# Optimization experiments

Measured on AMD Instinct MI355X. Metric: run time of the kernel, lower is better.

Reference implementation:

```python
import jax, jax.numpy as jnp
import numpy as np

HIDDEN = 450
DEPTH = 4
ATOM_FDIM = 35
BOND_FDIM = 5
MAX_NB = 15
N_ATOMS = 30000
N_BONDS = 60000
N_MESS = 10001
N_MOLS = 1000
EPS = 1e-5


def setup_inputs() -> dict:
    key = jax.random.key(0)
    ks = jax.random.split(key, 10)
    fatoms = jax.random.normal(ks[0], (N_ATOMS, ATOM_FDIM), dtype=jnp.float32)
    fbonds = jax.random.normal(ks[1], (N_BONDS, ATOM_FDIM + BOND_FDIM), dtype=jnp.float32)
    # indices into concatenated [tree_message; graph_message] table (index 0 = zero pad slot)
    agraph = jax.random.randint(ks[2], (N_ATOMS, MAX_NB), 0, N_MESS + N_BONDS)
    bgraph = jax.random.randint(ks[3], (N_BONDS, MAX_NB), 0, N_MESS + N_BONDS)
    per_mol = N_ATOMS // N_MOLS
    starts = jnp.arange(N_MOLS, dtype=jnp.int64) * per_mol
    lens = jnp.full((N_MOLS,), per_mol, dtype=jnp.int64)
    scope = jnp.stack([starts, lens], axis=1)
    tree_message = jax.random.normal(ks[4], (N_MESS, HIDDEN), dtype=jnp.float32)
    tree_message = tree_message.at[0].set(0.0)  # padding row
    s = 0.05
    W_i = jax.random.normal(ks[5], (HIDDEN, ATOM_FDIM + BOND_FDIM), dtype=jnp.float32) * s
    W_h = jax.random.normal(ks[6], (HIDDEN, HIDDEN), dtype=jnp.float32) * s
    W_o = jax.random.normal(ks[7], (HIDDEN, ATOM_FDIM + HIDDEN), dtype=jnp.float32) * s
    b_o = jax.random.normal(ks[8], (HIDDEN,), dtype=jnp.float32) * s
    gamma = jnp.ones((HIDDEN,), dtype=jnp.float32)
    beta = jnp.zeros((HIDDEN,), dtype=jnp.float32)
    return {"fatoms": fatoms, "fbonds": fbonds, "agraph": agraph, "bgraph": bgraph,
            "scope": scope, "tree_message": tree_message, "W_i": W_i, "W_h": W_h,
            "W_o": W_o, "b_o": b_o, "gamma": gamma, "beta": beta}


def reference(fatoms, fbonds, agraph, bgraph, scope, tree_message, W_i, W_h, W_o, b_o, gamma, beta):
    # bond input features -> hidden
    binput = fbonds @ W_i.T                      # [n_bonds, H]
    graph_message = jax.nn.relu(binput)
    # message-passing loop (dropout is identity in eval / p=0)
    for _ in range(DEPTH - 1):
        message = jnp.concatenate([tree_message, graph_message], axis=0)
        nei = message[bgraph].sum(axis=1)        # padded-neighbor gather + sum -> [n_bonds, H]
        graph_message = jax.nn.relu(binput + nei @ W_h.T)
    message = jnp.concatenate([tree_message, graph_message], axis=0)
    nei = message[agraph].sum(axis=1)            # [n_atoms, H]
    ainput = jnp.concatenate([fatoms, nei], axis=1)
    h = ainput @ W_o.T + b_o                     # [n_atoms, H]
    # BatchNorm1d (training-mode batch statistics, biased variance)
    mean = h.mean(axis=0)
    var = ((h - mean) ** 2).mean(axis=0)
    h = (h - mean) * jax.lax.rsqrt(var + EPS) * gamma + beta
    h = jax.nn.relu(h)
    # scope-based segment mean pooling
    starts = scope[:, 0]
    lens = scope[:, 1]
    mol_id = jnp.searchsorted(starts, jnp.arange(N_ATOMS), side="right") - 1
    sums = jax.ops.segment_sum(h, mol_id, num_segments=N_MOLS)
    denom = jnp.maximum(lens, 1).astype(h.dtype)[:, None]
    return jnp.where(lens[:, None] > 0, sums / denom, jnp.zeros_like(sums))
```

## Files before the change

kernel.cpp:

```cpp
#include <hip/hip_runtime.h>
#include <cstdint>
#include <cstddef>

#define HIDDEN 450
#define ATOM_FDIM 35
#define IN_FDIM 40
#define MAX_NB 15
#define N_ATOMS 30000
#define N_BONDS 60000
#define N_MESS 10001
#define N_MOLS 1000
#define DEPTH 4
#define NTOT (N_MESS + N_BONDS)

#define KPAD 512
#define MB_PAD 60032
#define MA_PAD 30080

typedef _Float16 f16x8_t __attribute__((ext_vector_type(8)));
typedef float f32x4_t __attribute__((ext_vector_type(4)));
typedef unsigned short ushort8_t __attribute__((ext_vector_type(8)));

__device__ __forceinline__ float h2f(unsigned short u) {
    return (float)__builtin_bit_cast(_Float16, u);
}
__device__ __forceinline__ unsigned short f2h(float f) {
    return __builtin_bit_cast(unsigned short, (_Float16)f);
}
__device__ __forceinline__ void st_out(unsigned short* p, float v) { *p = f2h(v); }
__device__ __forceinline__ void st_out(float* p, float v) { *p = v; }

__device__ __forceinline__ void g2l16(const unsigned short* g, unsigned short* l) {
    __builtin_amdgcn_global_load_lds(
        (const __attribute__((address_space(1))) void*)g,
        (__attribute__((address_space(3))) void*)l, 16, 0, 0);
}

__device__ __forceinline__ bool sniff_is64(const void* g) {
    const int* g32 = (const int*)g;
    return (g32[1] | g32[3] | g32[5] | g32[7]) == 0;
}
__device__ __forceinline__ long long load_idx(const void* g, size_t pos, bool is64) {
    return is64 ? ((const long long*)g)[pos] : (long long)((const int*)g)[pos];
}

__global__ void prep_w_kernel(const float* __restrict__ W_i,
                              const float* __restrict__ W_h,
                              const float* __restrict__ W_o,
                              unsigned short* __restrict__ Wih,
                              unsigned short* __restrict__ Wo) {
    int t = blockIdx.x * blockDim.x + threadIdx.x;
    if (t < KPAD * KPAD) {
        int n = t >> 9, k = t & 511;
        float v = 0.f;
        if (n < HIDDEN) {
            if (k < IN_FDIM)               v = W_i[(size_t)n * IN_FDIM + k];
            else if (k < IN_FDIM + HIDDEN) v = W_h[(size_t)n * HIDDEN + (k - IN_FDIM)];
        }
        Wih[t] = f2h(v);
    } else if (t < 2 * KPAD * KPAD) {
        int u = t - KPAD * KPAD;
        int n = u >> 9, k = u & 511;
        float v = 0.f;
        if (n < HIDDEN) {
            if (k < ATOM_FDIM) v = W_o[(size_t)n * (ATOM_FDIM + HIDDEN) + k];
            else if (k >= IN_FDIM && k < IN_FDIM + HIDDEN)
                v = W_o[(size_t)n * (ATOM_FDIM + HIDDEN) + ATOM_FDIM + (k - IN_FDIM)];
        }
        Wo[u] = f2h(v);
    }
}

#define PR_B0 (MB_PAD * 10)
#define PR_B1 (PR_B0 + MA_PAD * 7)
#define PR_B2 (PR_B1 + N_MESS * 64)
#define PR_B3 (PR_B2 + N_BONDS * 8)
#define PR_B4 (PR_B3 + 1024)
__global__ void prep_data_kernel(const float* __restrict__ fbonds,
                                 const float* __restrict__ fatoms,
                                 const float* __restrict__ tree,
                                 unsigned short* __restrict__ Ab,
                                 unsigned short* __restrict__ Aa,
                                 unsigned short* __restrict__ tb,
                                 unsigned short* __restrict__ gm,
                                 float* __restrict__ stats) {
    for (int t = blockIdx.x * blockDim.x + threadIdx.x; t < PR_B4;
         t += gridDim.x * blockDim.x) {
        if (t < PR_B0) {
            int r = t / 10, c = t % 10;
            int col0 = (c < 8) ? c * 8 : 496 + (c - 8) * 8;
            ushort8_t o;
            #pragma unroll
            for (int j = 0; j < 8; ++j) {
                int cc = col0 + j;
                float v = (r < N_BONDS && cc < IN_FDIM) ? fbonds[(size_t)r * IN_FDIM + cc] : 0.f;
                o[j] = f2h(v);
            }
            *(ushort8_t*)(Ab + (size_t)r * KPAD + col0) = o;
        } else if (t < PR_B1) {
            int u = t - PR_B0;
            int r = u / 7, c = u % 7;
            int col0 = (c < 5) ? c * 8 : 496 + (c - 5) * 8;
            ushort8_t o;
            #pragma unroll
            for (int j = 0; j < 8; ++j) {
                int cc = col0 + j;
                float v = (r < N_ATOMS && cc < ATOM_FDIM) ? fatoms[(size_t)r * ATOM_FDIM + cc] : 0.f;
                o[j] = f2h(v);
            }
            *(ushort8_t*)(Aa + (size_t)r * KPAD + col0) = o;
        } else if (t < PR_B2) {
            int u = t - PR_B1;
            int r = u >> 6, c8 = (u & 63) * 8;
            ushort8_t o;
            #pragma unroll
            for (int j = 0; j < 8; ++j) {
                int c = c8 + j;
                float v = (c < HIDDEN) ? tree[(size_t)r * HIDDEN + c] : 0.f;
                o[j] = f2h(v);
            }
            *(ushort8_t*)(tb + (size_t)r * KPAD + c8) = o;
        } else if (t < PR_B3) {
            int u = t - PR_B2;
            int r = u >> 3, c = 448 + (u & 7) * 8;
            ushort8_t z = {0, 0, 0, 0, 0, 0, 0, 0};
            *(ushort8_t*)(gm + (size_t)r * KPAD + c) = z;
        } else {
            int i = t - PR_B3;
            if (i < 2 * HIDDEN) stats[i] = 0.f;
        }
    }
}

template<bool RELU, bool BIAS, bool CSTAT, typename OT>
__global__ __launch_bounds__(256)
void mfma_gemm_kernel(const unsigned short* __restrict__ A,
                      const unsigned short* __restrict__ B,
                      const float* __restrict__ bias,
                      OT* __restrict__ Out, int ldo,
                      int M, int Nvalid, int K, int mtiles,
                      float* __restrict__ sums, float* __restrict__ sumsq)
{
    __shared__ unsigned short As[2][128 * 32];
    __shared__ unsigned short Bs[2][128 * 32];
    const int g = blockIdx.x;
    const int mt = (g >> 5) * 8 + (g & 7);
    const int nt = (g >> 3) & 3;
    if (mt >= mtiles) return;
    const int m0 = mt * 128, n0 = nt * 128;

    const int tid  = threadIdx.x;
    const int wave = tid >> 6, lane = tid & 63;
    const int wm = wave >> 1, wn = wave & 1;

    const unsigned short* At = A + (size_t)m0 * KPAD;
    const unsigned short* Bt = B + (size_t)n0 * KPAD;

    const int c0 = wave * 128 + lane;
    const int c1 = c0 + 64;
    const int rA0 = c0 >> 2, kc0 = (c0 & 3) * 8;
    const int rA1 = c1 >> 2, kc1 = (c1 & 3) * 8;
    const int lofs0 = (wave * 128) * 8;
    const int lofs1 = (wave * 128 + 64) * 8;

    const int fr = lane & 15, kof = (lane >> 4) * 8;

    f32x4_t acc[4][4];
    #pragma unroll
    for (int mi = 0; mi < 4; ++mi)
        #pragma unroll
        for (int ni = 0; ni < 4; ++ni)
            acc[mi][ni] = f32x4_t{0.f, 0.f, 0.f, 0.f};

    auto stage = [&](int buf, int k0) {
        g2l16(At + (size_t)rA0 * KPAD + k0 + kc0, &As[buf][lofs0]);
        g2l16(At + (size_t)rA1 * KPAD + k0 + kc1, &As[buf][lofs1]);
        g2l16(Bt + (size_t)rA0 * KPAD + k0 + kc0, &Bs[buf][lofs0]);
        g2l16(Bt + (size_t)rA1 * KPAD + k0 + kc1, &Bs[buf][lofs1]);
    };
    auto compute = [&](int buf) {
        f16x8_t a[4], b[4];
        #pragma unroll
        for (int mi = 0; mi < 4; ++mi)
            a[mi] = __builtin_bit_cast(f16x8_t,
                *(const ushort8_t*)&As[buf][(size_t)((wm * 64 + mi * 16 + fr) * 32 + kof)]);
        #pragma unroll
        for (int ni = 0; ni < 4; ++ni)
            b[ni] = __builtin_bit_cast(f16x8_t,
                *(const ushort8_t*)&Bs[buf][(size_t)((wn * 64 + ni * 16 + fr) * 32 + kof)]);
        #pragma unroll
        for (int mi = 0; mi < 4; ++mi)
            #pragma unroll
            for (int ni = 0; ni < 4; ++ni)
                acc[mi][ni] = __builtin_amdgcn_mfma_f32_16x16x32_f16(
                    a[mi], b[ni], acc[mi][ni], 0, 0, 0);
    };

    stage(0, 0);
    __syncthreads();
    int cur = 0;
    for (int k0 = 32; k0 < K; k0 += 32) {
        stage(cur ^ 1, k0);
        compute(cur);
        __syncthreads();
        cur ^= 1;
    }
    compute(cur);

    float cs[4] = {0.f, 0.f, 0.f, 0.f}, cq[4] = {0.f, 0.f, 0.f, 0.f};
    #pragma unroll
    for (int mi = 0; mi < 4; ++mi) {
        int row_b = m0 + wm * 64 + mi * 16 + (lane >> 4) * 4;
        #pragma unroll
        for (int ni = 0; ni < 4; ++ni) {
            int col = n0 + wn * 64 + ni * 16 + fr;
            if (col >= Nvalid) continue;
            float bi = BIAS ? bias[col] : 0.f;
            #pragma unroll
            for (int r = 0; r < 4; ++r) {
                int row = row_b + r;
                if (row >= M) continue;
                float v = acc[mi][ni][r] + bi;
                if (CSTAT) { cs[ni] += v; cq[ni] += v * v; }
                if (RELU) v = fmaxf(v, 0.f);
                st_out(&Out[(size_t)row * ldo + col], v);
            }
        }
    }
    if (CSTAT) {
        #pragma unroll
        for (int ni = 0; ni < 4; ++ni) {
            int col = n0 + wn * 64 + ni * 16 + fr;
            if (col < Nvalid) {
                atomicAdd(&sums[col], cs[ni]);
                atomicAdd(&sumsq[col], cq[ni]);
            }
        }
    }
}

__global__ __launch_bounds__(256)
void gather_kernel(const void* __restrict__ graph, int n_rows,
                   const unsigned short* __restrict__ tree,
                   const unsigned short* __restrict__ gm,
                   unsigned short* __restrict__ Adst)
{
    const bool is64 = sniff_is64(graph);
    int w    = (int)((blockIdx.x * 256 + threadIdx.x) >> 6);
    int lane = threadIdx.x & 63;
    if (w >= n_rows) return;
    const size_t coff = (size_t)lane * 8;

    const unsigned short* rp[MAX_NB];
    #pragma unroll
    for (int nb = 0; nb < MAX_NB; ++nb) {
        long long idx = load_idx(graph, (size_t)w * MAX_NB + nb, is64);
        if (idx < 0) idx = 0;
        if (idx >= NTOT) idx = NTOT - 1;
        int i32 = __builtin_amdgcn_readfirstlane((int)idx);
        rp[nb] = (i32 < N_MESS) ? tree + (size_t)i32 * KPAD
                                : gm + (size_t)(i32 - N_MESS) * KPAD;
    }
    ushort8_t v[MAX_NB];
    #pragma unroll
    for (int nb = 0; nb < MAX_NB; ++nb)
        v[nb] = *(const ushort8_t*)(rp[nb] + coff);

    float acc[8] = {};
    #pragma unroll
    for (int nb = 0; nb < MAX_NB; ++nb)
        #pragma unroll
        for (int j = 0; j < 8; ++j)
            acc[j] += h2f(v[nb][j]);

    if (lane < 57) {
        ushort8_t o;
        #pragma unroll
        for (int j = 0; j < 8; ++j) o[j] = f2h(acc[j]);
        *(ushort8_t*)(Adst + (size_t)w * KPAD + IN_FDIM + coff) = o;
    }
}

__global__ void finalize_stats_kernel(const float* __restrict__ sums,
                                      const float* __restrict__ sumsq,
                                      const float* __restrict__ gamma,
                                      const float* __restrict__ beta,
                                      float* __restrict__ scale,
                                      float* __restrict__ shift)
{
    int c = blockIdx.x * blockDim.x + threadIdx.x;
    if (c >= HIDDEN) return;
    float mean = sums[c] * (1.f / N_ATOMS);
    float var  = sumsq[c] * (1.f / N_ATOMS) - mean * mean;
    float inv  = rsqrtf(var + 1e-5f);
    float sc   = gamma[c] * inv;
    scale[c] = sc;
    shift[c] = beta[c] - mean * sc;
}

__global__ __launch_bounds__(256)
void pool_kernel(const unsigned short* __restrict__ h, const void* __restrict__ scope,
                 const float* __restrict__ scale, const float* __restrict__ shift,
                 float* __restrict__ out)
{
    int m = blockIdx.x;
    const int* s32 = (const int*)scope;
    bool is64 = (s32[1] == 0 && s32[3] == 0);
    long long start, len, nxt;
    if (is64) {
        const long long* s = (const long long*)scope;
        start = s[2 * m]; len = s[2 * m + 1];
        nxt = (m < N_MOLS - 1) ? s[2 * m + 2] : (long long)N_ATOMS;
    } else {
        start = s32[2 * m]; len = s32[2 * m + 1];
        nxt = (m < N_MOLS - 1) ? (long long)s32[2 * m + 2] : (long long)N_ATOMS;
    }
    if (start < 0) start = 0;
    if (nxt > N_ATOMS) nxt = N_ATOMS;

    int t = threadIdx.x;
    bool has1 = t < HIDDEN - 256;
    float sc0 = scale[t], sh0 = shift[t];
    float sc1 = 0.f, sh1 = 0.f;
    if (has1) { sc1 = scale[t + 256]; sh1 = shift[t + 256]; }
    float a0 = 0.f, a1 = 0.f;
    for (long long r = start; r < nxt; ++r) {
        const unsigned short* row = h + (size_t)r * HIDDEN;
        a0 += fmaxf(fmaf(h2f(row[t]), sc0, sh0), 0.f);
        if (has1) a1 += fmaxf(fmaf(h2f(row[t + 256]), sc1, sh1), 0.f);
    }
    float den = (float)(len > 0 ? len : 1);
    out[(size_t)m * HIDDEN + t] = (len > 0) ? a0 / den : 0.f;
    if (has1) out[(size_t)m * HIDDEN + t + 256] = (len > 0) ? a1 / den : 0.f;
}

extern "C" void kernel_launch(void* const* d_in, const int* in_sizes, int n_in,
                              void* d_out, int out_size, void* d_ws, size_t ws_size,
                              hipStream_t stream)
{
    const float* fatoms = (const float*)d_in[0];
    const float* fbonds = (const float*)d_in[1];
    const void*  agraph = d_in[2];
    const void*  bgraph = d_in[3];
    const void*  scope  = d_in[4];
    const float* tree   = (const float*)d_in[5];
    const float* W_i    = (const float*)d_in[6];
    const float* W_h    = (const float*)d_in[7];
    const float* W_o    = (const float*)d_in[8];
    const float* b_o    = (const float*)d_in[9];
    const float* gamma  = (const float*)d_in[10];
    const float* beta   = (const float*)d_in[11];
    float* out = (float*)d_out;

    char* ws = (char*)d_ws;
    size_t off = 0;
    auto alloc = [&](size_t bytes) { char* p = ws + off; off += (bytes + 255) & ~(size_t)255; return p; };
    float*          sums  = (float*)alloc(4 * HIDDEN * sizeof(float));
    float*          sumsq = sums + HIDDEN;
    float*          scale = sums + 2 * HIDDEN;
    float*          shift = sums + 3 * HIDDEN;
    unsigned short* Abond = (unsigned short*)alloc((size_t)MB_PAD * KPAD * 2);
    unsigned short* Aatom = (unsigned short*)alloc((size_t)MA_PAD * KPAD * 2);
    unsigned short* gm    = (unsigned short*)alloc((size_t)N_BONDS * KPAD * 2);
    unsigned short* tb    = (unsigned short*)alloc((size_t)N_MESS * KPAD * 2);
    unsigned short* Wih   = (unsigned short*)alloc((size_t)KPAD * KPAD * 2);
    unsigned short* Wo    = (unsigned short*)alloc((size_t)KPAD * KPAD * 2);
    unsigned short* h     = (unsigned short*)alloc((size_t)N_ATOMS * HIDDEN * 2);
    (void)ws_size;

    dim3 blk(256);

    prep_w_kernel<<<(2 * KPAD * KPAD + 255) / 256, blk, 0, stream>>>(W_i, W_h, W_o, Wih, Wo);
    prep_data_kernel<<<2048, blk, 0, stream>>>(fbonds, fatoms, tree, Abond, Aatom, tb, gm, sums);

    dim3 gBond(59 * 32);
    dim3 gAtom(30 * 32);

    mfma_gemm_kernel<true, false, false, unsigned short><<<gBond, blk, 0, stream>>>(
        Abond, Wih, nullptr, gm, KPAD, N_BONDS, HIDDEN, 64, 469, nullptr, nullptr);

    for (int it = 0; it < DEPTH - 1; ++it) {
        gather_kernel<<<N_BONDS / 4, blk, 0, stream>>>(bgraph, N_BONDS, tb, gm, Abond);
        mfma_gemm_kernel<true, false, false, unsigned short><<<gBond, blk, 0, stream>>>(
            Abond, Wih, nullptr, gm, KPAD, N_BONDS, HIDDEN, KPAD, 469, nullptr, nullptr);
    }

    gather_kernel<<<N_ATOMS / 4, blk, 0, stream>>>(agraph, N_ATOMS, tb, gm, Aatom);
    mfma_gemm_kernel<false, true, true, unsigned short><<<gAtom, blk, 0, stream>>>(
        Aatom, Wo, b_o, h, HIDDEN, N_ATOMS, HIDDEN, KPAD, 235, sums, sumsq);

    finalize_stats_kernel<<<1, 512, 0, stream>>>(sums, sumsq, gamma, beta, scale, shift);
    pool_kernel<<<N_MOLS, blk, 0, stream>>>(h, scope, scale, shift, out);
}
```

Baseline: 908.1 us.

## Replace double-buffered LDS staging with single buffer in MFMA GEMM

Removes the ping-pong LDS double buffering in the MFMA GEMM main loop and uses a single shared tile with two barriers per K-step. This halves shared memory per block, which may allow more resident blocks per CU and lower pointer arithmetic. In exchange, global-to-LDS loads no longer overlap with MFMA compute inside a block, so latency hiding depends on other resident blocks.

```diff
diff --git a/kernel.cpp b/kernel.cpp
--- a/kernel.cpp
+++ b/kernel.cpp
@@ -141,8 +141,8 @@
                       int M, int Nvalid, int K, int mtiles,
                       float* __restrict__ sums, float* __restrict__ sumsq)
 {
-    __shared__ unsigned short As[2][128 * 32];
-    __shared__ unsigned short Bs[2][128 * 32];
+    __shared__ unsigned short As[128 * 32];
+    __shared__ unsigned short Bs[128 * 32];
     const int g = blockIdx.x;
     const int mt = (g >> 5) * 8 + (g & 7);
     const int nt = (g >> 3) & 3;
@@ -160,8 +160,10 @@
     const int c1 = c0 + 64;
     const int rA0 = c0 >> 2, kc0 = (c0 & 3) * 8;
     const int rA1 = c1 >> 2, kc1 = (c1 & 3) * 8;
-    const int lofs0 = (wave * 128) * 8;
-    const int lofs1 = (wave * 128 + 64) * 8;
+    unsigned short* lA0 = &As[(size_t)(wave * 128) * 8];
+    unsigned short* lA1 = &As[(size_t)(wave * 128 + 64) * 8];
+    unsigned short* lB0 = &Bs[(size_t)(wave * 128) * 8];
+    unsigned short* lB1 = &Bs[(size_t)(wave * 128 + 64) * 8];
 
     const int fr = lane & 15, kof = (lane >> 4) * 8;
 
@@ -172,40 +174,30 @@
         for (int ni = 0; ni < 4; ++ni)
             acc[mi][ni] = f32x4_t{0.f, 0.f, 0.f, 0.f};
 
-    auto stage = [&](int buf, int k0) {
-        g2l16(At + (size_t)rA0 * KPAD + k0 + kc0, &As[buf][lofs0]);
-        g2l16(At + (size_t)rA1 * KPAD + k0 + kc1, &As[buf][lofs1]);
-        g2l16(Bt + (size_t)rA0 * KPAD + k0 + kc0, &Bs[buf][lofs0]);
-        g2l16(Bt + (size_t)rA1 * KPAD + k0 + kc1, &Bs[buf][lofs1]);
-    };
-    auto compute = [&](int buf) {
+    for (int k0 = 0; k0 < K; k0 += 32) {
+        g2l16(At + (size_t)rA0 * KPAD + k0 + kc0, lA0);
+        g2l16(At + (size_t)rA1 * KPAD + k0 + kc1, lA1);
+        g2l16(Bt + (size_t)rA0 * KPAD + k0 + kc0, lB0);
+        g2l16(Bt + (size_t)rA1 * KPAD + k0 + kc1, lB1);
+        __syncthreads();
+
         f16x8_t a[4], b[4];
         #pragma unroll
         for (int mi = 0; mi < 4; ++mi)
             a[mi] = __builtin_bit_cast(f16x8_t,
-                *(const ushort8_t*)&As[buf][(size_t)((wm * 64 + mi * 16 + fr) * 32 + kof)]);
+                *(const ushort8_t*)&As[(size_t)((wm * 64 + mi * 16 + fr) * 32 + kof)]);
         #pragma unroll
         for (int ni = 0; ni < 4; ++ni)
             b[ni] = __builtin_bit_cast(f16x8_t,
-                *(const ushort8_t*)&Bs[buf][(size_t)((wn * 64 + ni * 16 + fr) * 32 + kof)]);
+                *(const ushort8_t*)&Bs[(size_t)((wn * 64 + ni * 16 + fr) * 32 + kof)]);
         #pragma unroll
         for (int mi = 0; mi < 4; ++mi)
             #pragma unroll
             for (int ni = 0; ni < 4; ++ni)
                 acc[mi][ni] = __builtin_amdgcn_mfma_f32_16x16x32_f16(
                     a[mi], b[ni], acc[mi][ni], 0, 0, 0);
-    };
-
-    stage(0, 0);
-    __syncthreads();
-    int cur = 0;
-    for (int k0 = 32; k0 < K; k0 += 32) {
-        stage(cur ^ 1, k0);
-        compute(cur);
         __syncthreads();
-        cur ^= 1;
-    }
-    compute(cur);
+    }
 
     float cs[4] = {0.f, 0.f, 0.f, 0.f}, cq[4] = {0.f, 0.f, 0.f, 0.f};
     #pragma unroll
```

After: 909.2 us. About the same (+0.1%).
